# Performance work log

Hardware: AMD Instinct MI355X
Metric: run time of the kernel (lower is better)

The kernel has to match this reference:

```python
import jax, jax.numpy as jnp
import numpy as np

N = 131072        # number of points
S = 16384         # number of groups (segments)
D_IN = 256        # fea_dims[0]
NUM_RF = 1024     # random-feature width
D_OUT = 128       # fea_dims[1] (embedding dim)
_INV_SQRT2 = 1.0 / np.sqrt(2.0).astype(np.float32)
_INV_SQRT2PI = 1.0 / np.sqrt(2.0 * np.pi).astype(np.float32)


def setup_inputs() -> dict:
    key = jax.random.key(0)
    k1, k2, k3, k4, k5, k6 = jax.random.split(key, 6)
    X = jax.random.normal(k1, (N, D_IN), dtype=jnp.float32)
    # balanced group assignment (guarantees no empty segment -> no inf/nan)
    X_idx = jax.random.permutation(k2, jnp.arange(N, dtype=jnp.int64) % S)
    W1_mu = jax.random.normal(k3, (NUM_RF, D_IN), dtype=jnp.float32) * 0.05
    W1_var = jax.random.uniform(k4, (NUM_RF, D_IN), dtype=jnp.float32) * 0.01 + 1e-4
    W2_mu = jax.random.normal(k5, (D_OUT, NUM_RF), dtype=jnp.float32) * 0.05
    W2_var = jax.random.uniform(k6, (D_OUT, NUM_RF), dtype=jnp.float32) * 0.01 + 1e-4
    return {"X": X, "X_idx": X_idx, "W1_mu": W1_mu, "W1_var": W1_var,
            "W2_mu": W2_mu, "W2_var": W2_var}


def _vb_linear(m, v, W_mu, W_var):
    # Variational Bayes linear layer: propagate mean/variance through
    # independent Gaussian weights W ~ N(W_mu, W_var).
    mo = m @ W_mu.T                                   # [N, out]
    if v is None:
        vo = (m * m) @ W_var.T
    else:
        vo = v @ (W_mu * W_mu).T + (m * m + v) @ W_var.T
    return mo, vo


def _relu_moments(mu, var):
    # Exact first/second moments of ReLU of a Gaussian N(mu, var).
    s = jnp.sqrt(var + 1e-8)
    z = mu / s
    Phi = 0.5 * (1.0 + jax.scipy.special.erf(z * _INV_SQRT2))
    phi = jnp.exp(-0.5 * z * z) * _INV_SQRT2PI
    m_out = mu * Phi + s * phi
    e_y2 = (mu * mu + var) * Phi + mu * s * phi
    v_out = jnp.maximum(e_y2 - m_out * m_out, 1e-6)
    return m_out, v_out


def reference(X, X_idx, W1_mu, W1_var, W2_mu, W2_var):
    # DGP-RF block: D_IN -> NUM_RF (ReLU moments) -> D_OUT
    m, v = _vb_linear(X, None, W1_mu, W1_var)         # [N, NUM_RF]
    m, v = _relu_moments(m, v)
    out_means, out_vars = _vb_linear(m, v, W2_mu, W2_var)  # [N, D_OUT]
    # Precision-weighted aggregation over X_idx groups (Gaussian product)
    prec = 1.0 / out_vars                              # [N, D_OUT]
    embedd_vars = 1.0 / jax.ops.segment_sum(prec, X_idx, num_segments=S)
    embedd_means = jax.ops.segment_sum(prec * out_means, X_idx, num_segments=S)
    embedd_means = embedd_means * embedd_vars          # [S, D_OUT]
    return embedd_means, embedd_vars
```

## Files before the change

### kernel.cpp

```cpp
#include <hip/hip_runtime.h>


#define NPTS   131072
#define SGRP   16384
#define DIN    256
#define NRF    1024
#define DOUT   128
#define MT     64
#define NWG    (NPTS / MT)

#define XLD    264
#define TLD    136

typedef __attribute__((ext_vector_type(8))) short bf16x8;
typedef __attribute__((ext_vector_type(4))) float f32x4;
typedef __attribute__((ext_vector_type(2))) float f32x2;
typedef __attribute__((ext_vector_type(4))) float f32x4v;

__device__ __forceinline__ unsigned short f2bf(float f) {
  unsigned u = __float_as_uint(f);
  u += 0x7fffu + ((u >> 16) & 1u);
  return (unsigned short)(u >> 16);
}

__device__ __forceinline__ float fast_rcp(float x) {
#if __has_builtin(__builtin_amdgcn_rcpf)
  return __builtin_amdgcn_rcpf(x);
#else
  return 1.0f / x;
#endif
}
__device__ __forceinline__ float fast_rsq(float x) {
#if __has_builtin(__builtin_amdgcn_rsqf)
  return __builtin_amdgcn_rsqf(x);
#else
  return rsqrtf(x);
#endif
}
__device__ __forceinline__ float fast_exp2(float x) {
#if __has_builtin(__builtin_amdgcn_exp2f)
  return __builtin_amdgcn_exp2f(x);
#else
  return exp2f(x);
#endif
}

__device__ __forceinline__ bf16x8 sq_frag(bf16x8 a) {
  union { bf16x8 h; unsigned u[4]; } in, out;
  in.h = a;
#pragma unroll
  for (int i = 0; i < 4; ++i) {
    unsigned w = in.u[i];
    f32x2 f;
    f[0] = __uint_as_float(w << 16);
    f[1] = __uint_as_float(w & 0xffff0000u);
    f32x2 s = f * f;
    unsigned lo = (__float_as_uint(s[0]) + 0x8000u) >> 16;
    unsigned hi = (__float_as_uint(s[1]) + 0x8000u) & 0xffff0000u;
    out.u[i] = hi | lo;
  }
  return out.h;
}

__device__ __forceinline__ void relu_moments(float mu, float v,
                                             float& mo, float& vo) {
  float vpe = v + 1e-8f;
  float rsq = fast_rsq(vpe);
  float s   = vpe * rsq;
  float z   = mu * rsq;
  float E   = fast_exp2(-0.7213475204444817f * z * z);
  float x   = 0.70710678118654752f * fabsf(z);
  float t   = fast_rcp(fmaf(0.3275911f, x, 1.0f));
  float poly = t * fmaf(t, fmaf(t, fmaf(t, fmaf(t, 1.061405429f, -1.453152027f),
                                        1.421413741f), -0.284496736f), 0.254829592f);
  float q   = 0.5f * poly * E;
  float Phi = (z >= 0.0f) ? (1.0f - q) : q;
  float phi = 0.3989422804014327f * E;
  float sphi = s * phi;
  mo = fmaf(mu, Phi, sphi);
  float ey2 = fmaf(fmaf(mu, mu, v), Phi, mu * sphi);
  vo = fmaxf(fmaf(-mo, mo, ey2), 1e-6f);
}

__global__ void detect_idx_kernel(const unsigned* __restrict__ raw,
                                  int* __restrict__ flag) {
  __shared__ int any_nz;
  if (threadIdx.x == 0) any_nz = 0;
  __syncthreads();
  if (raw[2 * threadIdx.x + 1] != 0u) atomicOr(&any_nz, 1);
  __syncthreads();
  if (threadIdx.x == 0) *flag = (any_nz == 0) ? 1 : 0;
}

__global__ __launch_bounds__(256) void convert_kernel(
    const float* __restrict__ W1mu, const float* __restrict__ W1var,
    const float* __restrict__ W2mu, const float* __restrict__ W2var,
    unsigned short* __restrict__ w1mu_bf, unsigned short* __restrict__ w1var_bf,
    unsigned short* __restrict__ w2mu_bf, unsigned short* __restrict__ w2b_bf,
    unsigned short* __restrict__ w2var_bf) {
  int i = blockIdx.x * 256 + threadIdx.x;
  w1mu_bf[i]  = f2bf(W1mu[i]);
  w1var_bf[i] = f2bf(W1var[i]);
  if (i < NRF * DOUT) {
    float m = W2mu[i];
    float v = W2var[i];
    w2mu_bf[i]  = f2bf(m);
    w2b_bf[i]   = f2bf(fmaf(m, m, v));
    w2var_bf[i] = f2bf(v);
  }
}

__global__ __launch_bounds__(256, 2) void fused_kernel(
    const float* __restrict__ X,
    const unsigned* __restrict__ Xidx_raw,
    const unsigned short* __restrict__ W1mu, const unsigned short* __restrict__ W1var,
    const unsigned short* __restrict__ W2mu, const unsigned short* __restrict__ W2b,
    const unsigned short* __restrict__ W2var,
    const int* __restrict__ flag64,
    float* __restrict__ acc_means,
    float* __restrict__ acc_vars) {
  __shared__ unsigned short Xb[MT * XLD];
  __shared__ unsigned short Tm[MT * TLD];
  __shared__ unsigned short Tv[MT * TLD];
  __shared__ int sidx[MT];

  const int tid = threadIdx.x;
  const int p0  = blockIdx.x * MT;
  const int is64 = *flag64;

  if (tid < MT) {
    int p = p0 + tid;
    sidx[tid] = (int)(is64 ? Xidx_raw[2 * (size_t)p] : Xidx_raw[p]);
  }
#pragma unroll
  for (int i = 0; i < 16; ++i) {
    int idx4 = i * 256 + tid;
    int row  = idx4 >> 6;
    int c4   = idx4 & 63;
    f32x4v xv = *(const f32x4v*)(X + (size_t)(p0 + row) * DIN + c4 * 4);
    int off = row * XLD + c4 * 4;
    ushort4 b;
    b.x = f2bf(xv[0]); b.y = f2bf(xv[1]); b.z = f2bf(xv[2]); b.w = f2bf(xv[3]);
    *(ushort4*)(Xb + off) = b;
  }
  __syncthreads();

  const int lane = tid & 63;
  const int wave = tid >> 6;
  const int l16  = lane & 15;
  const int quad = lane >> 4;
  const int qoff = quad * 8;

  const int nrow0 = (wave * 2 + 0) * 16 + l16;
  const int nrow1 = (wave * 2 + 1) * 16 + l16;

  f32x4 acc_mo[4][2], acc_vo[4][2];
#pragma unroll
  for (int mt = 0; mt < 4; ++mt)
#pragma unroll
    for (int j = 0; j < 2; ++j) {
      acc_mo[mt][j] = (f32x4){0.f, 0.f, 0.f, 0.f};
      acc_vo[mt][j] = (f32x4){0.f, 0.f, 0.f, 0.f};
    }

  bf16x8 g1mu[2][2], g1vr[2][2];
#pragma unroll
  for (int k = 0; k < 2; ++k) {
    size_t o0 = (size_t)nrow0 * DIN + k * 32 + qoff;
    size_t o1 = (size_t)nrow1 * DIN + k * 32 + qoff;
    g1mu[k][0] = *(const bf16x8*)(W1mu + o0);
    g1mu[k][1] = *(const bf16x8*)(W1mu + o1);
    g1vr[k][0] = *(const bf16x8*)(W1var + o0);
    g1vr[k][1] = *(const bf16x8*)(W1var + o1);
  }

#pragma unroll 1
  for (int c = 0; c < 8; ++c) {
    f32x4 am[4][2], av[4][2];
#pragma unroll
    for (int mt = 0; mt < 4; ++mt)
#pragma unroll
      for (int nt = 0; nt < 2; ++nt) {
        am[mt][nt] = (f32x4){0.f, 0.f, 0.f, 0.f};
        av[mt][nt] = (f32x4){0.f, 0.f, 0.f, 0.f};
      }
    const size_t cbase1 = (size_t)(c * 128) * DIN;
#pragma unroll
    for (int k = 0; k < 8; ++k) {
      bf16x8 cmu0 = g1mu[k & 1][0], cmu1 = g1mu[k & 1][1];
      bf16x8 cvr0 = g1vr[k & 1][0], cvr1 = g1vr[k & 1][1];
      if (k < 6) {
        size_t o0 = cbase1 + (size_t)nrow0 * DIN + (k + 2) * 32 + qoff;
        size_t o1 = cbase1 + (size_t)nrow1 * DIN + (k + 2) * 32 + qoff;
        g1mu[k & 1][0] = *(const bf16x8*)(W1mu + o0);
        g1mu[k & 1][1] = *(const bf16x8*)(W1mu + o1);
        g1vr[k & 1][0] = *(const bf16x8*)(W1var + o0);
        g1vr[k & 1][1] = *(const bf16x8*)(W1var + o1);
      }
#pragma unroll
      for (int mt = 0; mt < 4; ++mt) {
        bf16x8 ax = *(const bf16x8*)(Xb + (mt * 16 + l16) * XLD + k * 32 + qoff);
        bf16x8 aq = sq_frag(ax);
        am[mt][0] = __builtin_amdgcn_mfma_f32_16x16x32_bf16(ax, cmu0, am[mt][0], 0, 0, 0);
        am[mt][1] = __builtin_amdgcn_mfma_f32_16x16x32_bf16(ax, cmu1, am[mt][1], 0, 0, 0);
        av[mt][0] = __builtin_amdgcn_mfma_f32_16x16x32_bf16(aq, cvr0, av[mt][0], 0, 0, 0);
        av[mt][1] = __builtin_amdgcn_mfma_f32_16x16x32_bf16(aq, cvr1, av[mt][1], 0, 0, 0);
      }
    }

    if (c < 7) {
      const size_t nbase1 = (size_t)((c + 1) * 128) * DIN;
#pragma unroll
      for (int k = 0; k < 2; ++k) {
        size_t o0 = nbase1 + (size_t)nrow0 * DIN + k * 32 + qoff;
        size_t o1 = nbase1 + (size_t)nrow1 * DIN + k * 32 + qoff;
        g1mu[k][0] = *(const bf16x8*)(W1mu + o0);
        g1mu[k][1] = *(const bf16x8*)(W1mu + o1);
        g1vr[k][0] = *(const bf16x8*)(W1var + o0);
        g1vr[k][1] = *(const bf16x8*)(W1var + o1);
      }
    }

    bf16x8 g2m[2][2], g2b[2][2], g2v[2][2];
    const size_t cbase2 = (size_t)(c * 128);
#pragma unroll
    for (int k2 = 0; k2 < 2; ++k2) {
      size_t o0 = (size_t)nrow0 * NRF + cbase2 + k2 * 32 + qoff;
      size_t o1 = (size_t)nrow1 * NRF + cbase2 + k2 * 32 + qoff;
      g2m[k2][0] = *(const bf16x8*)(W2mu + o0);
      g2m[k2][1] = *(const bf16x8*)(W2mu + o1);
      g2b[k2][0] = *(const bf16x8*)(W2b + o0);
      g2b[k2][1] = *(const bf16x8*)(W2b + o1);
      g2v[k2][0] = *(const bf16x8*)(W2var + o0);
      g2v[k2][1] = *(const bf16x8*)(W2var + o1);
    }

    __syncthreads();

#pragma unroll
    for (int mt = 0; mt < 4; ++mt)
#pragma unroll
      for (int nt = 0; nt < 2; ++nt) {
        int col = (wave * 2 + nt) * 16 + l16;
#pragma unroll
        for (int r = 0; r < 4; ++r) {
          float mo, vo;
          relu_moments(am[mt][nt][r], av[mt][nt][r], mo, vo);
          int o = (mt * 16 + quad * 4 + r) * TLD + col;
          Tm[o] = f2bf(mo); Tv[o] = f2bf(vo);
        }
      }
    __syncthreads();

#pragma unroll
    for (int k2 = 0; k2 < 4; ++k2) {
      bf16x8 c2m0 = g2m[k2 & 1][0], c2m1 = g2m[k2 & 1][1];
      bf16x8 c2b0 = g2b[k2 & 1][0], c2b1 = g2b[k2 & 1][1];
      bf16x8 c2v0 = g2v[k2 & 1][0], c2v1 = g2v[k2 & 1][1];
      if (k2 < 2) {
        size_t o0 = (size_t)nrow0 * NRF + cbase2 + (k2 + 2) * 32 + qoff;
        size_t o1 = (size_t)nrow1 * NRF + cbase2 + (k2 + 2) * 32 + qoff;
        g2m[k2][0] = *(const bf16x8*)(W2mu + o0);
        g2m[k2][1] = *(const bf16x8*)(W2mu + o1);
        g2b[k2][0] = *(const bf16x8*)(W2b + o0);
        g2b[k2][1] = *(const bf16x8*)(W2b + o1);
        g2v[k2][0] = *(const bf16x8*)(W2var + o0);
        g2v[k2][1] = *(const bf16x8*)(W2var + o1);
      }
#pragma unroll
      for (int mt = 0; mt < 4; ++mt) {
        int aoff = (mt * 16 + l16) * TLD + k2 * 32 + qoff;
        bf16x8 fam = *(const bf16x8*)(Tm + aoff);
        bf16x8 fav = *(const bf16x8*)(Tv + aoff);
        bf16x8 fsq = sq_frag(fam);
        acc_mo[mt][0] = __builtin_amdgcn_mfma_f32_16x16x32_bf16(fam, c2m0, acc_mo[mt][0], 0, 0, 0);
        acc_mo[mt][1] = __builtin_amdgcn_mfma_f32_16x16x32_bf16(fam, c2m1, acc_mo[mt][1], 0, 0, 0);
        acc_vo[mt][0] = __builtin_amdgcn_mfma_f32_16x16x32_bf16(fav, c2b0, acc_vo[mt][0], 0, 0, 0);
        acc_vo[mt][1] = __builtin_amdgcn_mfma_f32_16x16x32_bf16(fav, c2b1, acc_vo[mt][1], 0, 0, 0);
        acc_vo[mt][0] = __builtin_amdgcn_mfma_f32_16x16x32_bf16(fsq, c2v0, acc_vo[mt][0], 0, 0, 0);
        acc_vo[mt][1] = __builtin_amdgcn_mfma_f32_16x16x32_bf16(fsq, c2v1, acc_vo[mt][1], 0, 0, 0);
      }
    }
  }

#pragma unroll
  for (int mt = 0; mt < 4; ++mt)
#pragma unroll
    for (int j = 0; j < 2; ++j) {
      int dim = (wave * 2 + j) * 16 + l16;
#pragma unroll
      for (int r = 0; r < 4; ++r) {
        int prow = mt * 16 + quad * 4 + r;
        float mo = acc_mo[mt][j][r];
        float vo = acc_vo[mt][j][r];
        float prec = fast_rcp(vo);
        size_t o = (size_t)sidx[prow] * DOUT + dim;
        unsafeAtomicAdd(acc_means + o, prec * mo);
        unsafeAtomicAdd(acc_vars + o, prec);
      }
    }
}

__global__ __launch_bounds__(256) void finalize_kernel(float* __restrict__ means,
                                                       float* __restrict__ vars) {
  int i = blockIdx.x * 256 + threadIdx.x;
  float p  = vars[i];
  float pm = means[i];
  float var = 1.0f / p;
  means[i] = pm * var;
  vars[i]  = var;
}

extern "C" void kernel_launch(void* const* d_in, const int* in_sizes, int n_in,
                              void* d_out, int out_size, void* d_ws, size_t ws_size,
                              hipStream_t stream) {
  const float*    X     = (const float*)d_in[0];
  const unsigned* Xidx  = (const unsigned*)d_in[1];
  const float*    W1mu  = (const float*)d_in[2];
  const float*    W1var = (const float*)d_in[3];
  const float*    W2mu  = (const float*)d_in[4];
  const float*    W2var = (const float*)d_in[5];
  float* out = (float*)d_out;

  unsigned short* w1mu_bf  = (unsigned short*)d_ws;
  unsigned short* w1var_bf = w1mu_bf + NRF * DIN;
  unsigned short* w2mu_bf  = w1var_bf + NRF * DIN;
  unsigned short* w2b_bf   = w2mu_bf + NRF * DOUT;
  unsigned short* w2var_bf = w2b_bf + NRF * DOUT;
  int* flag = (int*)(w2var_bf + NRF * DOUT);

  hipMemsetAsync(d_out, 0, (size_t)out_size * sizeof(float), stream);
  detect_idx_kernel<<<1, 256, 0, stream>>>(Xidx, flag);
  convert_kernel<<<(NRF * DIN) / 256, 256, 0, stream>>>(
      W1mu, W1var, W2mu, W2var, w1mu_bf, w1var_bf, w2mu_bf, w2b_bf, w2var_bf);
  fused_kernel<<<NWG, 256, 0, stream>>>(
      X, Xidx, w1mu_bf, w1var_bf, w2mu_bf, w2b_bf, w2var_bf, flag,
      out, out + (size_t)SGRP * DOUT);
  finalize_kernel<<<(SGRP * DOUT) / 256, 256, 0, stream>>>(
      out, out + (size_t)SGRP * DOUT);
}
```

Measured before the change: 714.9 us.

## Precompute bf16 X and X^2 in a pre-pass and stream A-fragments from global

Adds a pre-kernel that converts X to bf16 and also stores bf16 X squared in workspace. The fused kernel then loads these A-fragments straight from global memory with double-buffered register prefetch, instead of staging X in LDS and squaring it every chunk. This removes the X LDS buffer, which frees shared memory, and the launch bound is raised to 3 blocks per CU. The costs are an extra pass that writes 2x64MB, re-reading X fragments from global or L2 for all 8 chunks, and a dependence on workspace size, with a fallback to the old kernel when it is too small.

```diff
diff --git a/kernel.cpp b/kernel.cpp
--- a/kernel.cpp
+++ b/kernel.cpp
@@ -12,6 +12,7 @@
 #define XLD    264
 #define TLD    136
 
+typedef unsigned short ushort_t;
 typedef __attribute__((ext_vector_type(8))) short bf16x8;
 typedef __attribute__((ext_vector_type(4))) float f32x4;
 typedef __attribute__((ext_vector_type(2))) float f32x2;
@@ -95,9 +96,9 @@
 __global__ __launch_bounds__(256) void convert_kernel(
     const float* __restrict__ W1mu, const float* __restrict__ W1var,
     const float* __restrict__ W2mu, const float* __restrict__ W2var,
-    unsigned short* __restrict__ w1mu_bf, unsigned short* __restrict__ w1var_bf,
-    unsigned short* __restrict__ w2mu_bf, unsigned short* __restrict__ w2b_bf,
-    unsigned short* __restrict__ w2var_bf) {
+    ushort_t* __restrict__ w1mu_bf, ushort_t* __restrict__ w1var_bf,
+    ushort_t* __restrict__ w2mu_bf, ushort_t* __restrict__ w2b_bf,
+    ushort_t* __restrict__ w2var_bf) {
   int i = blockIdx.x * 256 + threadIdx.x;
   w1mu_bf[i]  = f2bf(W1mu[i]);
   w1var_bf[i] = f2bf(W1var[i]);
@@ -110,18 +111,236 @@
   }
 }
 
-__global__ __launch_bounds__(256, 2) void fused_kernel(
+__global__ __launch_bounds__(256) void xprep_kernel(
+    const float* __restrict__ X,
+    ushort_t* __restrict__ xbf, ushort_t* __restrict__ xsq) {
+  size_t i = ((size_t)blockIdx.x * 256 + threadIdx.x) * 4;
+  f32x4v x = *(const f32x4v*)(X + i);
+  ushort4 b, q;
+  b.x = f2bf(x[0]); b.y = f2bf(x[1]); b.z = f2bf(x[2]); b.w = f2bf(x[3]);
+  q.x = f2bf(x[0] * x[0]); q.y = f2bf(x[1] * x[1]);
+  q.z = f2bf(x[2] * x[2]); q.w = f2bf(x[3] * x[3]);
+  *(ushort4*)(xbf + i) = b;
+  *(ushort4*)(xsq + i) = q;
+}
+
+__global__ __launch_bounds__(256, 3) void fused_gx(
+    const ushort_t* __restrict__ Xbf, const ushort_t* __restrict__ Xsq,
+    const unsigned* __restrict__ Xidx_raw,
+    const ushort_t* __restrict__ W1mu, const ushort_t* __restrict__ W1var,
+    const ushort_t* __restrict__ W2mu, const ushort_t* __restrict__ W2b,
+    const ushort_t* __restrict__ W2var,
+    const int* __restrict__ flag64,
+    float* __restrict__ acc_means, float* __restrict__ acc_vars) {
+  __shared__ ushort_t Tm[MT * TLD];
+  __shared__ ushort_t Tv[MT * TLD];
+  __shared__ int sidx[MT];
+
+  const int tid = threadIdx.x;
+  const int p0  = blockIdx.x * MT;
+  const int is64 = *flag64;
+
+  if (tid < MT) {
+    int p = p0 + tid;
+    sidx[tid] = (int)(is64 ? Xidx_raw[2 * (size_t)p] : Xidx_raw[p]);
+  }
+
+  const int lane = tid & 63;
+  const int wave = tid >> 6;
+  const int l16  = lane & 15;
+  const int quad = lane >> 4;
+  const int qoff = quad * 8;
+
+  const int nrow0 = (wave * 2 + 0) * 16 + l16;
+  const int nrow1 = (wave * 2 + 1) * 16 + l16;
+
+  const ushort_t* pA[4];
+  const ushort_t* pQ[4];
+#pragma unroll
+  for (int mt = 0; mt < 4; ++mt) {
+    size_t ro = (size_t)(p0 + mt * 16 + l16) * DIN + qoff;
+    pA[mt] = Xbf + ro;
+    pQ[mt] = Xsq + ro;
+  }
+
+  f32x4 acc_mo[4][2], acc_vo[4][2];
+#pragma unroll
+  for (int mt = 0; mt < 4; ++mt)
+#pragma unroll
+    for (int j = 0; j < 2; ++j) {
+      acc_mo[mt][j] = (f32x4){0.f, 0.f, 0.f, 0.f};
+      acc_vo[mt][j] = (f32x4){0.f, 0.f, 0.f, 0.f};
+    }
+
+  bf16x8 axb[2][4], aqb[2][4];
+#pragma unroll
+  for (int mt = 0; mt < 4; ++mt) {
+    axb[0][mt] = *(const bf16x8*)(pA[mt]);
+    aqb[0][mt] = *(const bf16x8*)(pQ[mt]);
+  }
+
+  bf16x8 g1mu[2][2], g1vr[2][2];
+  {
+    const ushort_t* b0 = W1mu + (size_t)nrow0 * DIN + qoff;
+    const ushort_t* b1 = W1mu + (size_t)nrow1 * DIN + qoff;
+    const ushort_t* v0 = W1var + (size_t)nrow0 * DIN + qoff;
+    const ushort_t* v1 = W1var + (size_t)nrow1 * DIN + qoff;
+#pragma unroll
+    for (int k = 0; k < 2; ++k) {
+      g1mu[k][0] = *(const bf16x8*)(b0 + k * 32);
+      g1mu[k][1] = *(const bf16x8*)(b1 + k * 32);
+      g1vr[k][0] = *(const bf16x8*)(v0 + k * 32);
+      g1vr[k][1] = *(const bf16x8*)(v1 + k * 32);
+    }
+  }
+
+#pragma unroll 1
+  for (int c = 0; c < 8; ++c) {
+    const ushort_t* w1m0 = W1mu + ((size_t)(c * 128) + nrow0) * DIN + qoff;
+    const ushort_t* w1m1 = W1mu + ((size_t)(c * 128) + nrow1) * DIN + qoff;
+    const ushort_t* w1v0 = W1var + ((size_t)(c * 128) + nrow0) * DIN + qoff;
+    const ushort_t* w1v1 = W1var + ((size_t)(c * 128) + nrow1) * DIN + qoff;
+
+    f32x4 am[4][2], av[4][2];
+#pragma unroll
+    for (int mt = 0; mt < 4; ++mt)
+#pragma unroll
+      for (int nt = 0; nt < 2; ++nt) {
+        am[mt][nt] = (f32x4){0.f, 0.f, 0.f, 0.f};
+        av[mt][nt] = (f32x4){0.f, 0.f, 0.f, 0.f};
+      }
+
+#pragma unroll
+    for (int k = 0; k < 8; ++k) {
+      const int cur = k & 1, nxt = cur ^ 1;
+      bf16x8 cmu0 = g1mu[cur][0], cmu1 = g1mu[cur][1];
+      bf16x8 cvr0 = g1vr[cur][0], cvr1 = g1vr[cur][1];
+      if (k < 6) {
+        g1mu[cur][0] = *(const bf16x8*)(w1m0 + (k + 2) * 32);
+        g1mu[cur][1] = *(const bf16x8*)(w1m1 + (k + 2) * 32);
+        g1vr[cur][0] = *(const bf16x8*)(w1v0 + (k + 2) * 32);
+        g1vr[cur][1] = *(const bf16x8*)(w1v1 + (k + 2) * 32);
+      }
+      const int kn = (k + 1) & 7;
+#pragma unroll
+      for (int mt = 0; mt < 4; ++mt) {
+        axb[nxt][mt] = *(const bf16x8*)(pA[mt] + kn * 32);
+        aqb[nxt][mt] = *(const bf16x8*)(pQ[mt] + kn * 32);
+      }
+#pragma unroll
+      for (int mt = 0; mt < 4; ++mt) {
+        bf16x8 ax = axb[cur][mt];
+        bf16x8 aq = aqb[cur][mt];
+        am[mt][0] = __builtin_amdgcn_mfma_f32_16x16x32_bf16(ax, cmu0, am[mt][0], 0, 0, 0);
+        am[mt][1] = __builtin_amdgcn_mfma_f32_16x16x32_bf16(ax, cmu1, am[mt][1], 0, 0, 0);
+        av[mt][0] = __builtin_amdgcn_mfma_f32_16x16x32_bf16(aq, cvr0, av[mt][0], 0, 0, 0);
+        av[mt][1] = __builtin_amdgcn_mfma_f32_16x16x32_bf16(aq, cvr1, av[mt][1], 0, 0, 0);
+      }
+    }
+
+    if (c < 7) {
+#pragma unroll
+      for (int k = 0; k < 2; ++k) {
+        g1mu[k][0] = *(const bf16x8*)(w1m0 + 128 * DIN + k * 32);
+        g1mu[k][1] = *(const bf16x8*)(w1m1 + 128 * DIN + k * 32);
+        g1vr[k][0] = *(const bf16x8*)(w1v0 + 128 * DIN + k * 32);
+        g1vr[k][1] = *(const bf16x8*)(w1v1 + 128 * DIN + k * 32);
+      }
+    }
+
+    const ushort_t* w2m0 = W2mu + (size_t)nrow0 * NRF + c * 128 + qoff;
+    const ushort_t* w2m1 = W2mu + (size_t)nrow1 * NRF + c * 128 + qoff;
+    const ushort_t* w2b0 = W2b + (size_t)nrow0 * NRF + c * 128 + qoff;
+    const ushort_t* w2b1 = W2b + (size_t)nrow1 * NRF + c * 128 + qoff;
+    const ushort_t* w2v0 = W2var + (size_t)nrow0 * NRF + c * 128 + qoff;
+    const ushort_t* w2v1 = W2var + (size_t)nrow1 * NRF + c * 128 + qoff;
+    bf16x8 g2m[2][2], g2b[2][2], g2v[2][2];
+#pragma unroll
+    for (int k2 = 0; k2 < 2; ++k2) {
+      g2m[k2][0] = *(const bf16x8*)(w2m0 + k2 * 32);
+      g2m[k2][1] = *(const bf16x8*)(w2m1 + k2 * 32);
+      g2b[k2][0] = *(const bf16x8*)(w2b0 + k2 * 32);
+      g2b[k2][1] = *(const bf16x8*)(w2b1 + k2 * 32);
+      g2v[k2][0] = *(const bf16x8*)(w2v0 + k2 * 32);
+      g2v[k2][1] = *(const bf16x8*)(w2v1 + k2 * 32);
+    }
+
+    __syncthreads();
+
+#pragma unroll
+    for (int mt = 0; mt < 4; ++mt)
+#pragma unroll
+      for (int nt = 0; nt < 2; ++nt) {
+        int col = (wave * 2 + nt) * 16 + l16;
+#pragma unroll
+        for (int r = 0; r < 4; ++r) {
+          float mo, vo;
+          relu_moments(am[mt][nt][r], av[mt][nt][r], mo, vo);
+          int o = (mt * 16 + quad * 4 + r) * TLD + col;
+          Tm[o] = f2bf(mo); Tv[o] = f2bf(vo);
+        }
+      }
+    __syncthreads();
+
+#pragma unroll
+    for (int k2 = 0; k2 < 4; ++k2) {
+      const int cur2 = k2 & 1;
+      bf16x8 c2m0 = g2m[cur2][0], c2m1 = g2m[cur2][1];
+      bf16x8 c2b0 = g2b[cur2][0], c2b1 = g2b[cur2][1];
+      bf16x8 c2v0 = g2v[cur2][0], c2v1 = g2v[cur2][1];
+      if (k2 < 2) {
+        g2m[k2][0] = *(const bf16x8*)(w2m0 + (k2 + 2) * 32);
+        g2m[k2][1] = *(const bf16x8*)(w2m1 + (k2 + 2) * 32);
+        g2b[k2][0] = *(const bf16x8*)(w2b0 + (k2 + 2) * 32);
+        g2b[k2][1] = *(const bf16x8*)(w2b1 + (k2 + 2) * 32);
+        g2v[k2][0] = *(const bf16x8*)(w2v0 + (k2 + 2) * 32);
+        g2v[k2][1] = *(const bf16x8*)(w2v1 + (k2 + 2) * 32);
+      }
+#pragma unroll
+      for (int mt = 0; mt < 4; ++mt) {
+        int aoff = (mt * 16 + l16) * TLD + k2 * 32 + qoff;
+        bf16x8 fam = *(const bf16x8*)(Tm + aoff);
+        bf16x8 fav = *(const bf16x8*)(Tv + aoff);
+        bf16x8 fsq = sq_frag(fam);
+        acc_mo[mt][0] = __builtin_amdgcn_mfma_f32_16x16x32_bf16(fam, c2m0, acc_mo[mt][0], 0, 0, 0);
+        acc_mo[mt][1] = __builtin_amdgcn_mfma_f32_16x16x32_bf16(fam, c2m1, acc_mo[mt][1], 0, 0, 0);
+        acc_vo[mt][0] = __builtin_amdgcn_mfma_f32_16x16x32_bf16(fav, c2b0, acc_vo[mt][0], 0, 0, 0);
+        acc_vo[mt][1] = __builtin_amdgcn_mfma_f32_16x16x32_bf16(fav, c2b1, acc_vo[mt][1], 0, 0, 0);
+        acc_vo[mt][0] = __builtin_amdgcn_mfma_f32_16x16x32_bf16(fsq, c2v0, acc_vo[mt][0], 0, 0, 0);
+        acc_vo[mt][1] = __builtin_amdgcn_mfma_f32_16x16x32_bf16(fsq, c2v1, acc_vo[mt][1], 0, 0, 0);
+      }
+    }
+  }
+
+#pragma unroll
+  for (int mt = 0; mt < 4; ++mt)
+#pragma unroll
+    for (int j = 0; j < 2; ++j) {
+      int dim = (wave * 2 + j) * 16 + l16;
+#pragma unroll
+      for (int r = 0; r < 4; ++r) {
+        int prow = mt * 16 + quad * 4 + r;
+        float mo = acc_mo[mt][j][r];
+        float vo = acc_vo[mt][j][r];
+        float prec = fast_rcp(vo);
+        size_t o = (size_t)sidx[prow] * DOUT + dim;
+        unsafeAtomicAdd(acc_means + o, prec * mo);
+        unsafeAtomicAdd(acc_vars + o, prec);
+      }
+    }
+}
+
+__global__ __launch_bounds__(256, 2) void fused_fb(
     const float* __restrict__ X,
     const unsigned* __restrict__ Xidx_raw,
-    const unsigned short* __restrict__ W1mu, const unsigned short* __restrict__ W1var,
-    const unsigned short* __restrict__ W2mu, const unsigned short* __restrict__ W2b,
-    const unsigned short* __restrict__ W2var,
+    const ushort_t* __restrict__ W1mu, const ushort_t* __restrict__ W1var,
+    const ushort_t* __restrict__ W2mu, const ushort_t* __restrict__ W2b,
+    const ushort_t* __restrict__ W2var,
     const int* __restrict__ flag64,
-    float* __restrict__ acc_means,
-    float* __restrict__ acc_vars) {
-  __shared__ unsigned short Xb[MT * XLD];
-  __shared__ unsigned short Tm[MT * TLD];
-  __shared__ unsigned short Tv[MT * TLD];
+    float* __restrict__ acc_means, float* __restrict__ acc_vars) {
+  __shared__ ushort_t Xb[MT * XLD];
+  __shared__ ushort_t Tm[MT * TLD];
+  __shared__ ushort_t Tv[MT * TLD];
   __shared__ int sidx[MT];
 
   const int tid = threadIdx.x;
@@ -150,7 +369,6 @@
   const int l16  = lane & 15;
   const int quad = lane >> 4;
   const int qoff = quad * 8;
-
   const int nrow0 = (wave * 2 + 0) * 16 + l16;
   const int nrow1 = (wave * 2 + 1) * 16 + l16;
 
@@ -207,7 +425,6 @@
         av[mt][1] = __builtin_amdgcn_mfma_f32_16x16x32_bf16(aq, cvr1, av[mt][1], 0, 0, 0);
       }
     }
-
     if (c < 7) {
       const size_t nbase1 = (size_t)((c + 1) * 128) * DIN;
 #pragma unroll
@@ -220,7 +437,6 @@
         g1vr[k][1] = *(const bf16x8*)(W1var + o1);
       }
     }
-
     bf16x8 g2m[2][2], g2b[2][2], g2v[2][2];
     const size_t cbase2 = (size_t)(c * 128);
 #pragma unroll
@@ -234,9 +450,7 @@
       g2v[k2][0] = *(const bf16x8*)(W2var + o0);
       g2v[k2][1] = *(const bf16x8*)(W2var + o1);
     }
-
     __syncthreads();
-
 #pragma unroll
     for (int mt = 0; mt < 4; ++mt)
 #pragma unroll
@@ -251,7 +465,6 @@
         }
       }
     __syncthreads();
-
 #pragma unroll
     for (int k2 = 0; k2 < 4; ++k2) {
       bf16x8 c2m0 = g2m[k2 & 1][0], c2m1 = g2m[k2 & 1][1];
@@ -282,7 +495,6 @@
       }
     }
   }
-
 #pragma unroll
   for (int mt = 0; mt < 4; ++mt)
 #pragma unroll
@@ -322,20 +534,34 @@
   const float*    W2var = (const float*)d_in[5];
   float* out = (float*)d_out;
 
-  unsigned short* w1mu_bf  = (unsigned short*)d_ws;
-  unsigned short* w1var_bf = w1mu_bf + NRF * DIN;
-  unsigned short* w2mu_bf  = w1var_bf + NRF * DIN;
-  unsigned short* w2b_bf   = w2mu_bf + NRF * DOUT;
-  unsigned short* w2var_bf = w2b_bf + NRF * DOUT;
+  ushort_t* w1mu_bf  = (ushort_t*)d_ws;
+  ushort_t* w1var_bf = w1mu_bf + NRF * DIN;
+  ushort_t* w2mu_bf  = w1var_bf + NRF * DIN;
+  ushort_t* w2b_bf   = w2mu_bf + NRF * DOUT;
+  ushort_t* w2var_bf = w2b_bf + NRF * DOUT;
   int* flag = (int*)(w2var_bf + NRF * DOUT);
+
+  const size_t xoff_bytes = 2u << 20;
+  const size_t xelems = (size_t)NPTS * DIN;
+  ushort_t* xbf = (ushort_t*)((char*)d_ws + xoff_bytes);
+  ushort_t* xsq = xbf + xelems;
+  const size_t need = xoff_bytes + 2 * xelems * sizeof(ushort_t);
 
   hipMemsetAsync(d_out, 0, (size_t)out_size * sizeof(float), stream);
   detect_idx_kernel<<<1, 256, 0, stream>>>(Xidx, flag);
   convert_kernel<<<(NRF * DIN) / 256, 256, 0, stream>>>(
       W1mu, W1var, W2mu, W2var, w1mu_bf, w1var_bf, w2mu_bf, w2b_bf, w2var_bf);
-  fused_kernel<<<NWG, 256, 0, stream>>>(
-      X, Xidx, w1mu_bf, w1var_bf, w2mu_bf, w2b_bf, w2var_bf, flag,
-      out, out + (size_t)SGRP * DOUT);
+
+  if (ws_size >= need) {
+    xprep_kernel<<<(int)(xelems / 4 / 256), 256, 0, stream>>>(X, xbf, xsq);
+    fused_gx<<<NWG, 256, 0, stream>>>(
+        xbf, xsq, Xidx, w1mu_bf, w1var_bf, w2mu_bf, w2b_bf, w2var_bf, flag,
+        out, out + (size_t)SGRP * DOUT);
+  } else {
+    fused_fb<<<NWG, 256, 0, stream>>>(
+        X, Xidx, w1mu_bf, w1var_bf, w2mu_bf, w2b_bf, w2var_bf, flag,
+        out, out + (size_t)SGRP * DOUT);
+  }
   finalize_kernel<<<(SGRP * DOUT) / 256, 256, 0, stream>>>(
       out, out + (size_t)SGRP * DOUT);
 }
```

After: 1.980 ms. +177.0%, slower.
